# Performance work log

Measured on AMD Instinct MI355X. Metric: run time of the kernel, lower is better.

Reference implementation:

```python
import jax, jax.numpy as jnp
import numpy as np

TEMPERATURE = 1.0

def _rope_cos_sin(T, D):
    # inv_freq over even indices 0..D step 2 -> D//2 freqs
    inv_freq = 1.0 / (10000.0 ** (jnp.arange(0, D, 2, dtype=jnp.float32) / D))
    t = jnp.arange(T, dtype=jnp.float32)
    freqs = jnp.einsum('i,j->ij', t, inv_freq)          # [T, D//2]
    emb = jnp.concatenate([freqs, freqs], axis=-1)      # [T, D]
    return jnp.cos(emb), jnp.sin(emb)                   # each [T, D]

def _apply_rope(x, cos, sin):
    # x: [B,H,T,D]; cos/sin: [T,D] broadcast over B,H
    D = x.shape[-1]
    half = D // 2
    x1, x2 = x[..., :half], x[..., half:2 * half]
    c = cos[None, None, :, :half]
    s = sin[None, None, :, :half]
    rot = jnp.concatenate([x1 * c - x2 * s, x1 * s + x2 * c], axis=-1)
    if D > 2 * half:
        rot = jnp.concatenate([rot, x[..., 2 * half:]], axis=-1)
    return rot

def setup_inputs() -> dict:
    key = jax.random.key(0)
    kq, kk, kv = jax.random.split(key, 3)
    B, H, T, D = 2, 16, 2048, 64
    return {
        'q': jax.random.normal(kq, (B, H, T, D), dtype=jnp.float32),
        'k': jax.random.normal(kk, (B, H, T, D), dtype=jnp.float32),
        'v': jax.random.normal(kv, (B, H, T, D), dtype=jnp.float32),
    }

def reference(q, k, v):
    B, H, T, D = q.shape
    cos, sin = _rope_cos_sin(T, D)
    qr = _apply_rope(q, cos, sin)
    kr = _apply_rope(k, cos, sin)
    scale = jnp.sqrt(jnp.float32(D)) * TEMPERATURE
    scores = jnp.einsum('bhtd,bhsd->bhts', qr, kr) / scale  # [B,H,T,T]
    # original subtracts row max then softmax; identical to stable softmax
    attn = jax.nn.softmax(scores, axis=-1)
    out = jnp.einsum('bhts,bhsd->bhtd', attn, v)
    return out, attn
```

## Files before the change

kernel.cpp:

```cpp
#include <hip/hip_runtime.h>
#include <hip/hip_bf16.h>
#include <math.h>


#define T_SEQ  2048
#define D_HEAD 64
#define BH_N   32
#define NCH    32
#define OUT_ELEMS (BH_N * T_SEQ * D_HEAD)

typedef __attribute__((ext_vector_type(8))) short bf16x8;
typedef __attribute__((ext_vector_type(4))) float f32x4;

__device__ __forceinline__ unsigned short f2bf(float x) {
    __hip_bfloat16 h = __float2bfloat16(x);
    return *reinterpret_cast<unsigned short*>(&h);
}

__device__ __forceinline__ int swz(int o) { return o ^ (((o >> 7) & 7) << 4); }
__device__ __forceinline__ int tswz(int row, int bcol) {
    return row * 256 + (bcol ^ ((row & 7) << 4));
}

__global__ void rope_table_kernel(float* __restrict__ ctab, float* __restrict__ stab) {
    int i = blockIdx.x * blockDim.x + threadIdx.x;
    if (i >= T_SEQ * 32) return;
    int t = i >> 5;
    int j = i & 31;
    float invf = powf(10000.0f, -(float)j / 32.0f);
    float a = (float)t * invf;
    ctab[i] = cosf(a);
    stab[i] = sinf(a);
}

__global__ __launch_bounds__(256)
void ropebf16_kernel(const float* __restrict__ Q, const float* __restrict__ K,
                     const float* __restrict__ ctab, const float* __restrict__ stab,
                     unsigned short* __restrict__ Qb, unsigned short* __restrict__ Kb,
                     float qscale)
{
    const int r  = blockIdx.x * 16 + (threadIdx.x >> 4);
    const int c4 = threadIdx.x & 15;
    const int t  = r & (T_SEQ - 1);
    const float* X = blockIdx.y ? K : Q;
    unsigned short* H = blockIdx.y ? Kb : Qb;
    const float scale = blockIdx.y ? 1.0f : qscale;
    const float4* xr = (const float4*)(X + (size_t)r * 64);
    float4 a = xr[c4];
    float4 b = xr[c4 ^ 8];
    float4 c = ((const float4*)(ctab + t * 32))[c4 & 7];
    float4 s = ((const float4*)(stab + t * 32))[c4 & 7];
    float4 ro;
    if (c4 < 8) {
        ro.x = a.x * c.x - b.x * s.x; ro.y = a.y * c.y - b.y * s.y;
        ro.z = a.z * c.z - b.z * s.z; ro.w = a.w * c.w - b.w * s.w;
    } else {
        ro.x = a.x * c.x + b.x * s.x; ro.y = a.y * c.y + b.y * s.y;
        ro.z = a.z * c.z + b.z * s.z; ro.w = a.w * c.w + b.w * s.w;
    }
    ushort4 h;
    h.x = f2bf(ro.x * scale); h.y = f2bf(ro.y * scale);
    h.z = f2bf(ro.z * scale); h.w = f2bf(ro.w * scale);
    *(ushort4*)(H + (size_t)r * 64 + c4 * 4) = h;
}

__global__ __launch_bounds__(256)
void vtbf16_kernel(const float* __restrict__ V, unsigned short* __restrict__ Vt)
{
    __shared__ float tile[64][65];
    const int bh = blockIdx.y;
    const int tt = blockIdx.x;
    const float* vg = V + ((size_t)bh * T_SEQ + tt * 64) * 64;
    #pragma unroll
    for (int i = 0; i < 4; ++i) {
        const int row = (threadIdx.x >> 4) + i * 16;
        const int c4  = threadIdx.x & 15;
        float4 a = *(const float4*)(vg + (size_t)row * 64 + c4 * 4);
        tile[row][c4 * 4 + 0] = a.x; tile[row][c4 * 4 + 1] = a.y;
        tile[row][c4 * 4 + 2] = a.z; tile[row][c4 * 4 + 3] = a.w;
    }
    __syncthreads();
    #pragma unroll
    for (int i = 0; i < 4; ++i) {
        const int d   = (threadIdx.x >> 4) + i * 16;
        const int tc4 = threadIdx.x & 15;
        ushort4 h;
        h.x = f2bf(tile[tc4 * 4 + 0][d]);
        h.y = f2bf(tile[tc4 * 4 + 1][d]);
        h.z = f2bf(tile[tc4 * 4 + 2][d]);
        h.w = f2bf(tile[tc4 * 4 + 3][d]);
        *(ushort4*)(Vt + ((size_t)bh * 64 + d) * T_SEQ + tt * 64 + tc4 * 4) = h;
    }
}

__global__ __launch_bounds__(256, 4)
void attn_mfma_kernel(const unsigned short* __restrict__ Qb,
                      const unsigned short* __restrict__ Kb,
                      const unsigned short* __restrict__ Vt,
                      float* __restrict__ out, float* __restrict__ attn)
{
    __shared__ __align__(16) unsigned short kbuf[3][64][64];
    __shared__ __align__(16) float tbuf[4][16 * 64];

    const int tid  = threadIdx.x;
    const int lane = tid & 63;
    const int w    = tid >> 6;
    const int lrow = lane & 15;
    const int lgrp = lane >> 4;

    const int lid = blockIdx.x;
    const int vid = (lid & 7) * 128 + (lid >> 3);
    const int bh  = vid >> 5;
    const int m   = vid & 31;
    const int t0  = m * 64 + w * 16;

    const size_t base = (size_t)bh * T_SEQ * D_HEAD;
    const char* kgb = (const char*)(Kb + base);
    const unsigned short* vgb = Vt + (size_t)bh * 64 * T_SEQ;

    bf16x8 qf0, qf1;
    {
        const unsigned short* qp = Qb + base + (size_t)(t0 + lrow) * 64 + lgrp * 8;
        qf0 = *(const bf16x8*)(qp);
        qf1 = *(const bf16x8*)(qp + 32);
    }

    const int so0 = w * 1024 + lane * 16;
    const int so1 = so0 + 4096;
    const int sq0 = swz(so0);
    const int sq1 = swz(so1);
    char* klds = (char*)&kbuf[0][0][0];
    char* tlds = (char*)&tbuf[w][0];

#define STAGE_K(b, cc) do { \
    __builtin_amdgcn_global_load_lds((const unsigned int*)(kgb + (size_t)(cc) * 8192 + sq0), \
        (unsigned int*)(klds + (b) * 8192 + w * 1024), 16, 0, 0); \
    __builtin_amdgcn_global_load_lds((const unsigned int*)(kgb + (size_t)(cc) * 8192 + sq1), \
        (unsigned int*)(klds + (b) * 8192 + 4096 + w * 1024), 16, 0, 0); \
} while (0)

    float rpa0 = 0.f, rpa1 = 0.f, rpa2 = 0.f, rpa3 = 0.f;
    STAGE_K(0, 0);
    STAGE_K(1, 1);
    for (int cc = 0; cc < NCH; ++cc) {
        if (cc < NCH - 1) { asm volatile("s_waitcnt vmcnt(2)" ::: "memory"); }
        else              { asm volatile("s_waitcnt vmcnt(0)" ::: "memory"); }
        __builtin_amdgcn_s_barrier();
        if (cc + 2 < NCH) STAGE_K((cc + 2) % 3, cc + 2);
        __builtin_amdgcn_sched_barrier(0);
        const char* kb = klds + (cc % 3) * 8192;
        #pragma unroll
        for (int nt = 0; nt < 4; ++nt) {
            const int o = (nt * 16 + lrow) * 128 + lgrp * 16;
            bf16x8 a0 = *(const bf16x8*)(kb + swz(o));
            bf16x8 a1 = *(const bf16x8*)(kb + swz(o + 64));
            f32x4 acc = (f32x4){0.f, 0.f, 0.f, 0.f};
            acc = __builtin_amdgcn_mfma_f32_16x16x32_bf16(a0, qf0, acc, 0, 0, 0);
            acc = __builtin_amdgcn_mfma_f32_16x16x32_bf16(a1, qf1, acc, 0, 0, 0);
            rpa0 += __builtin_amdgcn_exp2f(acc[0]);
            rpa1 += __builtin_amdgcn_exp2f(acc[1]);
            rpa2 += __builtin_amdgcn_exp2f(acc[2]);
            rpa3 += __builtin_amdgcn_exp2f(acc[3]);
        }
    }
    float rp = (rpa0 + rpa1) + (rpa2 + rpa3);
    rp += __shfl_xor(rp, 16, 64);
    rp += __shfl_xor(rp, 32, 64);
    const float inv = 1.0f / rp;

    __builtin_amdgcn_sched_barrier(0);
    __builtin_amdgcn_s_barrier();

    f32x4 o4[4];
    #pragma unroll
    for (int nd = 0; nd < 4; ++nd) o4[nd] = (f32x4){0.f, 0.f, 0.f, 0.f};

    float* abase = attn + (size_t)bh * T_SEQ * T_SEQ;

    STAGE_K(0, 0);
    STAGE_K(1, 1);
    bf16x8 vf[8];
    #pragma unroll
    for (int nd = 0; nd < 4; ++nd)
        #pragma unroll
        for (int ks = 0; ks < 2; ++ks)
            vf[nd * 2 + ks] = *(const bf16x8*)(vgb + (size_t)(nd * 16 + lrow) * T_SEQ
                                               + ks * 32 + lgrp * 8);
    asm volatile("s_waitcnt vmcnt(10)" ::: "memory");

    for (int cc = 0; cc < NCH; ++cc) {
        __builtin_amdgcn_s_barrier();
        __builtin_amdgcn_sched_barrier(0);

        const char* kb = klds + (cc % 3) * 8192;
        f32x4 s4[4];
        #pragma unroll
        for (int nt = 0; nt < 4; ++nt) {
            const int o = (nt * 16 + lrow) * 128 + lgrp * 16;
            bf16x8 a0 = *(const bf16x8*)(kb + swz(o));
            bf16x8 a1 = *(const bf16x8*)(kb + swz(o + 64));
            f32x4 acc = (f32x4){0.f, 0.f, 0.f, 0.f};
            acc = __builtin_amdgcn_mfma_f32_16x16x32_bf16(a0, qf0, acc, 0, 0, 0);
            acc = __builtin_amdgcn_mfma_f32_16x16x32_bf16(a1, qf1, acc, 0, 0, 0);
            s4[nt] = acc;
        }
        #pragma unroll
        for (int nt = 0; nt < 4; ++nt) {
            s4[nt][0] = __builtin_amdgcn_exp2f(s4[nt][0]) * inv;
            s4[nt][1] = __builtin_amdgcn_exp2f(s4[nt][1]) * inv;
            s4[nt][2] = __builtin_amdgcn_exp2f(s4[nt][2]) * inv;
            s4[nt][3] = __builtin_amdgcn_exp2f(s4[nt][3]) * inv;
        }
        #pragma unroll
        for (int nt = 0; nt < 4; ++nt)
            *(f32x4*)(tlds + tswz(lrow, (nt * 16 + lgrp * 4) * 4)) = s4[nt];
        asm volatile("s_waitcnt lgkmcnt(0)" ::: "memory");
        __builtin_amdgcn_sched_barrier(0);

        #pragma unroll
        for (int ks = 0; ks < 2; ++ks) {
            f32x4 pa0 = *(const f32x4*)(tlds + tswz(lrow, (ks * 32 + lgrp * 8) * 4));
            f32x4 pa1 = *(const f32x4*)(tlds + tswz(lrow, (ks * 32 + lgrp * 8 + 4) * 4));
            bf16x8 pa;
            pa[0] = (short)f2bf(pa0[0]); pa[1] = (short)f2bf(pa0[1]);
            pa[2] = (short)f2bf(pa0[2]); pa[3] = (short)f2bf(pa0[3]);
            pa[4] = (short)f2bf(pa1[0]); pa[5] = (short)f2bf(pa1[1]);
            pa[6] = (short)f2bf(pa1[2]); pa[7] = (short)f2bf(pa1[3]);
            #pragma unroll
            for (int nd = 0; nd < 4; ++nd)
                o4[nd] = __builtin_amdgcn_mfma_f32_16x16x32_bf16(pa, vf[nd * 2 + ks], o4[nd], 0, 0, 0);
        }
        f32x4 tr[4];
        #pragma unroll
        for (int i = 0; i < 4; ++i)
            tr[i] = *(const f32x4*)(tlds + tswz(i * 4 + (lane >> 4), (lane & 15) * 16));
        __builtin_amdgcn_sched_barrier(0);
        if (cc + 1 < NCH) {
            #pragma unroll
            for (int nd = 0; nd < 4; ++nd)
                #pragma unroll
                for (int ks = 0; ks < 2; ++ks)
                    vf[nd * 2 + ks] = *(const bf16x8*)(vgb + (size_t)(nd * 16 + lrow) * T_SEQ
                                                       + (cc + 1) * 64 + ks * 32 + lgrp * 8);
        }
        if (cc + 2 < NCH) STAGE_K((cc + 2) % 3, cc + 2);
        __builtin_amdgcn_sched_barrier(0);
        #pragma unroll
        for (int i = 0; i < 4; ++i)
            *(f32x4*)(abase + (size_t)(t0 + i * 4 + (lane >> 4)) * T_SEQ
                      + cc * 64 + (lane & 15) * 4) = tr[i];
        __builtin_amdgcn_sched_barrier(0);
        if (cc < NCH - 2)      { asm volatile("s_waitcnt vmcnt(18)" ::: "memory"); }
        else if (cc < NCH - 1) { asm volatile("s_waitcnt vmcnt(16)" ::: "memory"); }
    }

    #pragma unroll
    for (int nd = 0; nd < 4; ++nd)
        #pragma unroll
        for (int j = 0; j < 4; ++j)
            __builtin_nontemporal_store(o4[nd][j],
                out + base + (size_t)(t0 + lgrp * 4 + j) * D_HEAD + nd * 16 + lrow);

#undef STAGE_K
}

extern "C" void kernel_launch(void* const* d_in, const int* in_sizes, int n_in,
                              void* d_out, int out_size, void* d_ws, size_t ws_size,
                              hipStream_t stream) {
    const float* q = (const float*)d_in[0];
    const float* k = (const float*)d_in[1];
    const float* v = (const float*)d_in[2];
    float* out  = (float*)d_out;
    float* attn = out + (size_t)OUT_ELEMS;

    float* ctab = (float*)d_ws;
    float* stab = ctab + T_SEQ * 32;
    unsigned short* wsu = (unsigned short*)(stab + T_SEQ * 32);
    const size_t NE = (size_t)BH_N * T_SEQ * D_HEAD;
    unsigned short* Qb = wsu + 0 * NE;
    unsigned short* Kb = wsu + 1 * NE;
    unsigned short* Vt = wsu + 2 * NE;

    const float QSCALE = 0.18033688011112042f;

    rope_table_kernel<<<dim3((T_SEQ * 32 + 255) / 256), dim3(256), 0, stream>>>(ctab, stab);
    ropebf16_kernel<<<dim3(BH_N * T_SEQ / 16, 2), dim3(256), 0, stream>>>(q, k, ctab, stab, Qb, Kb, QSCALE);
    vtbf16_kernel<<<dim3(T_SEQ / 64, BH_N), dim3(256), 0, stream>>>(v, Vt);
    attn_mfma_kernel<<<dim3(BH_N * T_SEQ / 64), dim3(256), 0, stream>>>(Qb, Kb, Vt, out, attn);
}
```

Before: 227.7 us.

## Split key dimension across waves per 16-row query block with LDS reduction

Each block now handles 16 query rows instead of 64, and its four waves split the key dimension rather than the query rows. The kernel therefore launches four times as many blocks. The row-sum pass reads K straight from global memory per wave and combines partial sums through LDS. The main pass stages 128-key chunks with double buffering, and each wave computes a 32-key slice. Partial PV outputs are reduced across waves in LDS before the store, and attn stores become nontemporal. The aim is more parallelism and better-coalesced attn writes, at the cost of more block barriers, re-reading Q and K per block, and the cross-wave reduction.

Result: slower. 301.9 us (+32.6%).

```diff
diff --git a/kernel.cpp b/kernel.cpp
--- a/kernel.cpp
+++ b/kernel.cpp
@@ -6,7 +6,7 @@
 #define T_SEQ  2048
 #define D_HEAD 64
 #define BH_N   32
-#define NCH    32
+#define NIT    16
 #define OUT_ELEMS (BH_N * T_SEQ * D_HEAD)
 
 typedef __attribute__((ext_vector_type(8))) short bf16x8;
@@ -18,8 +18,8 @@
 }
 
 __device__ __forceinline__ int swz(int o) { return o ^ (((o >> 7) & 7) << 4); }
-__device__ __forceinline__ int tswz(int row, int bcol) {
-    return row * 256 + (bcol ^ ((row & 7) << 4));
+__device__ __forceinline__ int tswz(int row, int b) {
+    return row * 512 + (b ^ ((row & 7) << 4));
 }
 
 __global__ void rope_table_kernel(float* __restrict__ ctab, float* __restrict__ stab) {
@@ -99,8 +99,8 @@
                       const unsigned short* __restrict__ Vt,
                       float* __restrict__ out, float* __restrict__ attn)
 {
-    __shared__ __align__(16) unsigned short kbuf[3][64][64];
-    __shared__ __align__(16) float tbuf[4][16 * 64];
+    __shared__ __align__(16) unsigned short kbuf[2][128][64];
+    __shared__ __align__(16) float tbuf[16][128];
 
     const int tid  = threadIdx.x;
     const int lane = tid & 63;
@@ -109,13 +109,14 @@
     const int lgrp = lane >> 4;
 
     const int lid = blockIdx.x;
-    const int vid = (lid & 7) * 128 + (lid >> 3);
-    const int bh  = vid >> 5;
-    const int m   = vid & 31;
-    const int t0  = m * 64 + w * 16;
+    const int vid = (lid & 7) * 512 + (lid >> 3);
+    const int bh  = vid >> 7;
+    const int m   = vid & 127;
+    const int t0  = m * 16;
 
     const size_t base = (size_t)bh * T_SEQ * D_HEAD;
     const char* kgb = (const char*)(Kb + base);
+    const unsigned short* kgs = Kb + base;
     const unsigned short* vgb = Vt + (size_t)bh * 64 * T_SEQ;
 
     bf16x8 qf0, qf1;
@@ -125,51 +126,59 @@
         qf1 = *(const bf16x8*)(qp + 32);
     }
 
-    const int so0 = w * 1024 + lane * 16;
-    const int so1 = so0 + 4096;
-    const int sq0 = swz(so0);
-    const int sq1 = swz(so1);
-    char* klds = (char*)&kbuf[0][0][0];
-    char* tlds = (char*)&tbuf[w][0];
-
-#define STAGE_K(b, cc) do { \
-    __builtin_amdgcn_global_load_lds((const unsigned int*)(kgb + (size_t)(cc) * 8192 + sq0), \
-        (unsigned int*)(klds + (b) * 8192 + w * 1024), 16, 0, 0); \
-    __builtin_amdgcn_global_load_lds((const unsigned int*)(kgb + (size_t)(cc) * 8192 + sq1), \
-        (unsigned int*)(klds + (b) * 8192 + 4096 + w * 1024), 16, 0, 0); \
-} while (0)
-
     float rpa0 = 0.f, rpa1 = 0.f, rpa2 = 0.f, rpa3 = 0.f;
-    STAGE_K(0, 0);
-    STAGE_K(1, 1);
-    for (int cc = 0; cc < NCH; ++cc) {
-        if (cc < NCH - 1) { asm volatile("s_waitcnt vmcnt(2)" ::: "memory"); }
-        else              { asm volatile("s_waitcnt vmcnt(0)" ::: "memory"); }
-        __builtin_amdgcn_s_barrier();
-        if (cc + 2 < NCH) STAGE_K((cc + 2) % 3, cc + 2);
-        __builtin_amdgcn_sched_barrier(0);
-        const char* kb = klds + (cc % 3) * 8192;
+    for (int c = 0; c < 8; ++c) {
+        const int col0 = w * 512 + c * 64;
         #pragma unroll
         for (int nt = 0; nt < 4; ++nt) {
-            const int o = (nt * 16 + lrow) * 128 + lgrp * 16;
-            bf16x8 a0 = *(const bf16x8*)(kb + swz(o));
-            bf16x8 a1 = *(const bf16x8*)(kb + swz(o + 64));
+            const unsigned short* kp = kgs + (size_t)(col0 + nt * 16 + lrow) * 64 + lgrp * 8;
+            bf16x8 k0 = *(const bf16x8*)(kp);
+            bf16x8 k1 = *(const bf16x8*)(kp + 32);
             f32x4 acc = (f32x4){0.f, 0.f, 0.f, 0.f};
-            acc = __builtin_amdgcn_mfma_f32_16x16x32_bf16(a0, qf0, acc, 0, 0, 0);
-            acc = __builtin_amdgcn_mfma_f32_16x16x32_bf16(a1, qf1, acc, 0, 0, 0);
-            rpa0 += __builtin_amdgcn_exp2f(acc[0]);
-            rpa1 += __builtin_amdgcn_exp2f(acc[1]);
-            rpa2 += __builtin_amdgcn_exp2f(acc[2]);
-            rpa3 += __builtin_amdgcn_exp2f(acc[3]);
+            acc = __builtin_amdgcn_mfma_f32_16x16x32_bf16(k0, qf0, acc, 0, 0, 0);
+            acc = __builtin_amdgcn_mfma_f32_16x16x32_bf16(k1, qf1, acc, 0, 0, 0);
+            if (nt == 0) rpa0 += __builtin_amdgcn_exp2f(acc[0]) + __builtin_amdgcn_exp2f(acc[1])
+                               + __builtin_amdgcn_exp2f(acc[2]) + __builtin_amdgcn_exp2f(acc[3]);
+            if (nt == 1) rpa1 += __builtin_amdgcn_exp2f(acc[0]) + __builtin_amdgcn_exp2f(acc[1])
+                               + __builtin_amdgcn_exp2f(acc[2]) + __builtin_amdgcn_exp2f(acc[3]);
+            if (nt == 2) rpa2 += __builtin_amdgcn_exp2f(acc[0]) + __builtin_amdgcn_exp2f(acc[1])
+                               + __builtin_amdgcn_exp2f(acc[2]) + __builtin_amdgcn_exp2f(acc[3]);
+            if (nt == 3) rpa3 += __builtin_amdgcn_exp2f(acc[0]) + __builtin_amdgcn_exp2f(acc[1])
+                               + __builtin_amdgcn_exp2f(acc[2]) + __builtin_amdgcn_exp2f(acc[3]);
         }
     }
     float rp = (rpa0 + rpa1) + (rpa2 + rpa3);
     rp += __shfl_xor(rp, 16, 64);
     rp += __shfl_xor(rp, 32, 64);
-    const float inv = 1.0f / rp;
-
+    {
+        float* psum = &tbuf[0][0];
+        if (lane < 16) psum[w * 16 + lrow] = rp;
+    }
     __builtin_amdgcn_sched_barrier(0);
     __builtin_amdgcn_s_barrier();
+    const float inv = 1.0f / (tbuf[0][0 + lrow] + tbuf[0][16 + lrow]
+                            + tbuf[0][32 + lrow] + tbuf[0][48 + lrow]);
+    __builtin_amdgcn_sched_barrier(0);
+    __builtin_amdgcn_s_barrier();
+
+    char* klds = (char*)&kbuf[0][0][0];
+    char* tlds = (char*)&tbuf[0][0];
+    const int so0 = w * 4096 + lane * 16;
+    const int sq0 = swz(so0);
+    const int sq1 = swz(so0 + 1024);
+    const int sq2 = swz(so0 + 2048);
+    const int sq3 = swz(so0 + 3072);
+
+#define STAGE_K(b, cc) do { \
+    __builtin_amdgcn_global_load_lds((const unsigned int*)(kgb + (size_t)(cc) * 16384 + sq0), \
+        (unsigned int*)(klds + (b) * 16384 + so0), 16, 0, 0); \
+    __builtin_amdgcn_global_load_lds((const unsigned int*)(kgb + (size_t)(cc) * 16384 + sq1), \
+        (unsigned int*)(klds + (b) * 16384 + so0 + 1024), 16, 0, 0); \
+    __builtin_amdgcn_global_load_lds((const unsigned int*)(kgb + (size_t)(cc) * 16384 + sq2), \
+        (unsigned int*)(klds + (b) * 16384 + so0 + 2048), 16, 0, 0); \
+    __builtin_amdgcn_global_load_lds((const unsigned int*)(kgb + (size_t)(cc) * 16384 + sq3), \
+        (unsigned int*)(klds + (b) * 16384 + so0 + 3072), 16, 0, 0); \
+} while (0)
 
     f32x4 o4[4];
     #pragma unroll
@@ -178,25 +187,22 @@
     float* abase = attn + (size_t)bh * T_SEQ * T_SEQ;
 
     STAGE_K(0, 0);
-    STAGE_K(1, 1);
-    bf16x8 vf[8];
+    bf16x8 vf[4];
     #pragma unroll
     for (int nd = 0; nd < 4; ++nd)
-        #pragma unroll
-        for (int ks = 0; ks < 2; ++ks)
-            vf[nd * 2 + ks] = *(const bf16x8*)(vgb + (size_t)(nd * 16 + lrow) * T_SEQ
-                                               + ks * 32 + lgrp * 8);
-    asm volatile("s_waitcnt vmcnt(10)" ::: "memory");
-
-    for (int cc = 0; cc < NCH; ++cc) {
+        vf[nd] = *(const bf16x8*)(vgb + (size_t)(nd * 16 + lrow) * T_SEQ + w * 32 + lgrp * 8);
+    asm volatile("s_waitcnt vmcnt(4)" ::: "memory");
+
+    for (int cc = 0; cc < NIT; ++cc) {
         __builtin_amdgcn_s_barrier();
-        __builtin_amdgcn_sched_barrier(0);
-
-        const char* kb = klds + (cc % 3) * 8192;
-        f32x4 s4[4];
-        #pragma unroll
-        for (int nt = 0; nt < 4; ++nt) {
-            const int o = (nt * 16 + lrow) * 128 + lgrp * 16;
+        if (cc + 1 < NIT) STAGE_K((cc + 1) & 1, cc + 1);
+        __builtin_amdgcn_sched_barrier(0);
+
+        const char* kb = klds + (cc & 1) * 16384;
+        f32x4 s4[2];
+        #pragma unroll
+        for (int nt = 0; nt < 2; ++nt) {
+            const int o = (w * 32 + nt * 16 + lrow) * 128 + lgrp * 16;
             bf16x8 a0 = *(const bf16x8*)(kb + swz(o));
             bf16x8 a1 = *(const bf16x8*)(kb + swz(o + 64));
             f32x4 acc = (f32x4){0.f, 0.f, 0.f, 0.f};
@@ -205,22 +211,22 @@
             s4[nt] = acc;
         }
         #pragma unroll
-        for (int nt = 0; nt < 4; ++nt) {
+        for (int nt = 0; nt < 2; ++nt) {
             s4[nt][0] = __builtin_amdgcn_exp2f(s4[nt][0]) * inv;
             s4[nt][1] = __builtin_amdgcn_exp2f(s4[nt][1]) * inv;
             s4[nt][2] = __builtin_amdgcn_exp2f(s4[nt][2]) * inv;
             s4[nt][3] = __builtin_amdgcn_exp2f(s4[nt][3]) * inv;
         }
         #pragma unroll
-        for (int nt = 0; nt < 4; ++nt)
-            *(f32x4*)(tlds + tswz(lrow, (nt * 16 + lgrp * 4) * 4)) = s4[nt];
+        for (int nt = 0; nt < 2; ++nt)
+            *(f32x4*)(tlds + tswz(lrow, w * 128 + nt * 64 + lgrp * 16)) = s4[nt];
         asm volatile("s_waitcnt lgkmcnt(0)" ::: "memory");
         __builtin_amdgcn_sched_barrier(0);
 
-        #pragma unroll
-        for (int ks = 0; ks < 2; ++ks) {
-            f32x4 pa0 = *(const f32x4*)(tlds + tswz(lrow, (ks * 32 + lgrp * 8) * 4));
-            f32x4 pa1 = *(const f32x4*)(tlds + tswz(lrow, (ks * 32 + lgrp * 8 + 4) * 4));
+        {
+            const int b0 = w * 128 + lgrp * 32;
+            f32x4 pa0 = *(const f32x4*)(tlds + tswz(lrow, b0));
+            f32x4 pa1 = *(const f32x4*)(tlds + tswz(lrow, b0 + 16));
             bf16x8 pa;
             pa[0] = (short)f2bf(pa0[0]); pa[1] = (short)f2bf(pa0[1]);
             pa[2] = (short)f2bf(pa0[2]); pa[3] = (short)f2bf(pa0[3]);
@@ -228,38 +234,54 @@
             pa[6] = (short)f2bf(pa1[2]); pa[7] = (short)f2bf(pa1[3]);
             #pragma unroll
             for (int nd = 0; nd < 4; ++nd)
-                o4[nd] = __builtin_amdgcn_mfma_f32_16x16x32_bf16(pa, vf[nd * 2 + ks], o4[nd], 0, 0, 0);
-        }
-        f32x4 tr[4];
-        #pragma unroll
-        for (int i = 0; i < 4; ++i)
-            tr[i] = *(const f32x4*)(tlds + tswz(i * 4 + (lane >> 4), (lane & 15) * 16));
-        __builtin_amdgcn_sched_barrier(0);
-        if (cc + 1 < NCH) {
+                o4[nd] = __builtin_amdgcn_mfma_f32_16x16x32_bf16(pa, vf[nd], o4[nd], 0, 0, 0);
+        }
+        __builtin_amdgcn_sched_barrier(0);
+        __builtin_amdgcn_s_barrier();
+
+        const int r0 = w * 4 + (lane >> 5);
+        f32x4 tr0 = *(const f32x4*)(tlds + tswz(r0,     (lane & 31) * 16));
+        f32x4 tr1 = *(const f32x4*)(tlds + tswz(r0 + 2, (lane & 31) * 16));
+        asm volatile("s_waitcnt lgkmcnt(0)" ::: "memory");
+        __builtin_amdgcn_sched_barrier(0);
+        if (cc + 1 < NIT) {
             #pragma unroll
             for (int nd = 0; nd < 4; ++nd)
-                #pragma unroll
-                for (int ks = 0; ks < 2; ++ks)
-                    vf[nd * 2 + ks] = *(const bf16x8*)(vgb + (size_t)(nd * 16 + lrow) * T_SEQ
-                                                       + (cc + 1) * 64 + ks * 32 + lgrp * 8);
-        }
-        if (cc + 2 < NCH) STAGE_K((cc + 2) % 3, cc + 2);
-        __builtin_amdgcn_sched_barrier(0);
-        #pragma unroll
-        for (int i = 0; i < 4; ++i)
-            *(f32x4*)(abase + (size_t)(t0 + i * 4 + (lane >> 4)) * T_SEQ
-                      + cc * 64 + (lane & 15) * 4) = tr[i];
-        __builtin_amdgcn_sched_barrier(0);
-        if (cc < NCH - 2)      { asm volatile("s_waitcnt vmcnt(18)" ::: "memory"); }
-        else if (cc < NCH - 1) { asm volatile("s_waitcnt vmcnt(16)" ::: "memory"); }
-    }
-
+                vf[nd] = *(const bf16x8*)(vgb + (size_t)(nd * 16 + lrow) * T_SEQ
+                                          + (cc + 1) * 128 + w * 32 + lgrp * 8);
+        }
+        __builtin_amdgcn_sched_barrier(0);
+        __builtin_nontemporal_store(tr0,
+            (f32x4*)(abase + (size_t)(t0 + r0) * T_SEQ + cc * 128 + (lane & 31) * 4));
+        __builtin_nontemporal_store(tr1,
+            (f32x4*)(abase + (size_t)(t0 + r0 + 2) * T_SEQ + cc * 128 + (lane & 31) * 4));
+        __builtin_amdgcn_sched_barrier(0);
+        if (cc + 1 < NIT) { asm volatile("s_waitcnt vmcnt(6)" ::: "memory"); }
+    }
+
+    __builtin_amdgcn_sched_barrier(0);
+    __builtin_amdgcn_s_barrier();
+    float* pout = (float*)klds;
     #pragma unroll
     for (int nd = 0; nd < 4; ++nd)
         #pragma unroll
         for (int j = 0; j < 4; ++j)
-            __builtin_nontemporal_store(o4[nd][j],
-                out + base + (size_t)(t0 + lgrp * 4 + j) * D_HEAD + nd * 16 + lrow);
+            pout[w * 1024 + (lgrp * 4 + j) * 64 + nd * 16 + lrow] = o4[nd][j];
+    asm volatile("s_waitcnt lgkmcnt(0)" ::: "memory");
+    __builtin_amdgcn_sched_barrier(0);
+    __builtin_amdgcn_s_barrier();
+    {
+        const int r  = tid >> 4;
+        const int c4 = tid & 15;
+        f32x4 a = (f32x4){0.f, 0.f, 0.f, 0.f};
+        #pragma unroll
+        for (int ww = 0; ww < 4; ++ww) {
+            const f32x4 p = *(const f32x4*)(pout + ww * 1024 + r * 64 + c4 * 4);
+            a.x += p.x; a.y += p.y; a.z += p.z; a.w += p.w;
+        }
+        __builtin_nontemporal_store(a,
+            (f32x4*)(out + base + (size_t)(t0 + r) * D_HEAD + c4 * 4));
+    }
 
 #undef STAGE_K
 }
@@ -286,5 +308,5 @@
     rope_table_kernel<<<dim3((T_SEQ * 32 + 255) / 256), dim3(256), 0, stream>>>(ctab, stab);
     ropebf16_kernel<<<dim3(BH_N * T_SEQ / 16, 2), dim3(256), 0, stream>>>(q, k, ctab, stab, Qb, Kb, QSCALE);
     vtbf16_kernel<<<dim3(T_SEQ / 64, BH_N), dim3(256), 0, stream>>>(v, Vt);
-    attn_mfma_kernel<<<dim3(BH_N * T_SEQ / 64), dim3(256), 0, stream>>>(Qb, Kb, Vt, out, attn);
-}
+    attn_mfma_kernel<<<dim3(BH_N * T_SEQ / 16), dim3(256), 0, stream>>>(Qb, Kb, Vt, out, attn);
+}
```
